# Performance work log

Hardware: AMD Instinct MI355X
Metric: run time of the kernel (lower is better)

## Reference

```python
import jax, jax.numpy as jnp
import numpy as np

LOG_CLAMP = -100.0  # torch BCELoss clamps log terms at -100


def setup_inputs() -> dict:
    key = jax.random.key(0)
    k1, k2 = jax.random.split(key)
    N, C, H, W = 32, 1, 1024, 1024
    # predict must be in (0,1) for BCE; keep strictly inside via small eps margin
    predict = jax.random.uniform(k1, (N, C, H, W), dtype=jnp.float32, minval=1e-6, maxval=1.0 - 1e-6)
    target = jax.random.uniform(k2, (N, C, H, W), dtype=jnp.float32)
    return {"predict": predict, "target": target}


def reference(predict, target):
    # Original loops over (b, row, col) and sums nn.BCELoss() (mean over the C
    # channel vector) per pixel. Equivalent fused form:
    #   loss = sum_{b,h,w} mean_c [ -(t*log(p) + (1-t)*log(1-p)) ]
    log_p = jnp.maximum(jnp.log(predict), LOG_CLAMP)
    log_1mp = jnp.maximum(jnp.log1p(-predict), LOG_CLAMP)
    bce = -(target * log_p + (1.0 - target) * log_1mp)  # [N, C, H, W]
    return bce.mean(axis=1).sum()
```

## Files before the change

kernel.cpp:

```cpp
#include <hip/hip_runtime.h>


#define NB  2048
#define BLK 256

#define LOG2_CLAMP -144.26950408889634f
#define NEG_LN2    -0.6931471805599453f

__device__ __forceinline__ float bce4_log2(float4 p, float4 t) {
    float s, lp, l1;
    lp = fmaxf(__log2f(p.x),        LOG2_CLAMP);
    l1 = fmaxf(__log2f(1.0f - p.x), LOG2_CLAMP);
    s  = l1 + t.x * (lp - l1);
    lp = fmaxf(__log2f(p.y),        LOG2_CLAMP);
    l1 = fmaxf(__log2f(1.0f - p.y), LOG2_CLAMP);
    s += l1 + t.y * (lp - l1);
    lp = fmaxf(__log2f(p.z),        LOG2_CLAMP);
    l1 = fmaxf(__log2f(1.0f - p.z), LOG2_CLAMP);
    s += l1 + t.z * (lp - l1);
    lp = fmaxf(__log2f(p.w),        LOG2_CLAMP);
    l1 = fmaxf(__log2f(1.0f - p.w), LOG2_CLAMP);
    s += l1 + t.w * (lp - l1);
    return s;
}

__device__ __forceinline__ float block_reduce(float acc) {
    #pragma unroll
    for (int off = 32; off > 0; off >>= 1)
        acc += __shfl_down(acc, off, 64);
    __shared__ float wave_sums[4];
    int lane = threadIdx.x & 63;
    int wave = threadIdx.x >> 6;
    if (lane == 0) wave_sums[wave] = acc;
    __syncthreads();
    float s = 0.0f;
    if (wave == 0) {
        s = (lane < 4) ? wave_sums[lane] : 0.0f;
        #pragma unroll
        for (int off = 2; off > 0; off >>= 1)
            s += __shfl_down(s, off, 64);
    }
    return s;
}

__global__ void __launch_bounds__(BLK) bce_partial_kernel(
        const float4* __restrict__ p4,
        const float4* __restrict__ t4,
        float* __restrict__ partials,
        int n4) {
    const int chunk = n4 / gridDim.x;
    const int base  = blockIdx.x * chunk;

    float a0 = 0.f, a1 = 0.f, a2 = 0.f, a3 = 0.f,
          a4 = 0.f, a5 = 0.f, a6 = 0.f, a7 = 0.f;

    int o = 0;
    for (; o + 8 * BLK <= chunk; o += 8 * BLK) {
        int i = base + o + threadIdx.x;
        float4 p0 = p4[i];           float4 p1 = p4[i + 1 * BLK];
        float4 p2 = p4[i + 2 * BLK]; float4 p3 = p4[i + 3 * BLK];
        float4 p4v = p4[i + 4 * BLK]; float4 p5 = p4[i + 5 * BLK];
        float4 p6 = p4[i + 6 * BLK]; float4 p7 = p4[i + 7 * BLK];
        float4 t0 = t4[i];           float4 t1 = t4[i + 1 * BLK];
        float4 t2 = t4[i + 2 * BLK]; float4 t3 = t4[i + 3 * BLK];
        float4 t4v = t4[i + 4 * BLK]; float4 t5 = t4[i + 5 * BLK];
        float4 t6 = t4[i + 6 * BLK]; float4 t7 = t4[i + 7 * BLK];
        a0 += bce4_log2(p0, t0);  a1 += bce4_log2(p1, t1);
        a2 += bce4_log2(p2, t2);  a3 += bce4_log2(p3, t3);
        a4 += bce4_log2(p4v, t4v); a5 += bce4_log2(p5, t5);
        a6 += bce4_log2(p6, t6);  a7 += bce4_log2(p7, t7);
    }
    for (; o < chunk; o += BLK) {
        int i = base + o + threadIdx.x;
        if (o + (int)threadIdx.x < chunk)
            a0 += bce4_log2(p4[i], t4[i]);
    }
    if (blockIdx.x == 0) {
        for (int i = (int)gridDim.x * chunk + threadIdx.x; i < n4; i += BLK)
            a0 += bce4_log2(p4[i], t4[i]);
    }

    float s = block_reduce(((a0 + a1) + (a2 + a3)) + ((a4 + a5) + (a6 + a7)));
    if (threadIdx.x == 0)
        partials[blockIdx.x] = NEG_LN2 * s;
}

__global__ void __launch_bounds__(BLK) bce_final_kernel(
        const float* __restrict__ partials,
        float* __restrict__ out,
        int nb) {
    float acc = 0.0f;
    for (int i = threadIdx.x; i < nb; i += BLK)
        acc += partials[i];
    float s = block_reduce(acc);
    if (threadIdx.x == 0)
        out[0] = s;
}

__global__ void __launch_bounds__(BLK) bce_atomic_kernel(
        const float4* __restrict__ p4,
        const float4* __restrict__ t4,
        float* __restrict__ out,
        int n4) {
    const int tid    = blockIdx.x * blockDim.x + threadIdx.x;
    const int stride = gridDim.x * blockDim.x;
    float a = 0.0f;
    for (int i = tid; i < n4; i += stride)
        a += bce4_log2(p4[i], t4[i]);
    float s = block_reduce(a);
    if (threadIdx.x == 0)
        atomicAdd(out, NEG_LN2 * s);
}

extern "C" void kernel_launch(void* const* d_in, const int* in_sizes, int n_in,
                              void* d_out, int out_size, void* d_ws, size_t ws_size,
                              hipStream_t stream) {
    const float* predict = (const float*)d_in[0];
    const float* target  = (const float*)d_in[1];
    float* out = (float*)d_out;

    int n  = in_sizes[0];
    int n4 = n / 4;

    if (ws_size >= NB * sizeof(float) && n4 >= NB) {
        float* partials = (float*)d_ws;
        bce_partial_kernel<<<NB, BLK, 0, stream>>>(
            (const float4*)predict, (const float4*)target, partials, n4);
        bce_final_kernel<<<1, BLK, 0, stream>>>(partials, out, NB);
    } else {
        hipMemsetAsync(d_out, 0, sizeof(float), stream);
        bce_atomic_kernel<<<NB, BLK, 0, stream>>>(
            (const float4*)predict, (const float4*)target, out, n4);
    }
}
```

Baseline: 47.46 us.

## Fuse final reduction into partial kernel via hierarchical last-block atomic counters

Replaces the separate single-block final reduction kernel with a last-block-done pattern. Each block writes its partial, fences, and increments a per-group counter; the last block of each group bumps a global counter, and the very last block sums all partials. This removes one kernel launch and the gap between kernels, but adds a memset of the counter area each call plus atomics and fences at the end of every block.

```diff
diff --git a/kernel.cpp b/kernel.cpp
--- a/kernel.cpp
+++ b/kernel.cpp
@@ -1,8 +1,10 @@
 #include <hip/hip_runtime.h>
 
 
-#define NB  2048
-#define BLK 256
+#define NB     2048
+#define BLK    256
+#define GROUPS 64
+#define GRP_SHIFT 5
 
 #define LOG2_CLAMP -144.26950408889634f
 #define NEG_LN2    -0.6931471805599453f
@@ -43,10 +45,12 @@
     return s;
 }
 
-__global__ void __launch_bounds__(BLK) bce_partial_kernel(
+__global__ void __launch_bounds__(BLK) bce_fused_kernel(
         const float4* __restrict__ p4,
         const float4* __restrict__ t4,
         float* __restrict__ partials,
+        int* __restrict__ counters,
+        float* __restrict__ out,
         int n4) {
     const int chunk = n4 / gridDim.x;
     const int base  = blockIdx.x * chunk;
@@ -57,18 +61,18 @@
     int o = 0;
     for (; o + 8 * BLK <= chunk; o += 8 * BLK) {
         int i = base + o + threadIdx.x;
-        float4 p0 = p4[i];           float4 p1 = p4[i + 1 * BLK];
-        float4 p2 = p4[i + 2 * BLK]; float4 p3 = p4[i + 3 * BLK];
+        float4 p0 = p4[i];            float4 p1 = p4[i + 1 * BLK];
+        float4 p2 = p4[i + 2 * BLK];  float4 p3 = p4[i + 3 * BLK];
         float4 p4v = p4[i + 4 * BLK]; float4 p5 = p4[i + 5 * BLK];
-        float4 p6 = p4[i + 6 * BLK]; float4 p7 = p4[i + 7 * BLK];
-        float4 t0 = t4[i];           float4 t1 = t4[i + 1 * BLK];
-        float4 t2 = t4[i + 2 * BLK]; float4 t3 = t4[i + 3 * BLK];
+        float4 p6 = p4[i + 6 * BLK];  float4 p7 = p4[i + 7 * BLK];
+        float4 t0 = t4[i];            float4 t1 = t4[i + 1 * BLK];
+        float4 t2 = t4[i + 2 * BLK];  float4 t3 = t4[i + 3 * BLK];
         float4 t4v = t4[i + 4 * BLK]; float4 t5 = t4[i + 5 * BLK];
-        float4 t6 = t4[i + 6 * BLK]; float4 t7 = t4[i + 7 * BLK];
-        a0 += bce4_log2(p0, t0);  a1 += bce4_log2(p1, t1);
-        a2 += bce4_log2(p2, t2);  a3 += bce4_log2(p3, t3);
+        float4 t6 = t4[i + 6 * BLK];  float4 t7 = t4[i + 7 * BLK];
+        a0 += bce4_log2(p0, t0);   a1 += bce4_log2(p1, t1);
+        a2 += bce4_log2(p2, t2);   a3 += bce4_log2(p3, t3);
         a4 += bce4_log2(p4v, t4v); a5 += bce4_log2(p5, t5);
-        a6 += bce4_log2(p6, t6);  a7 += bce4_log2(p7, t7);
+        a6 += bce4_log2(p6, t6);   a7 += bce4_log2(p7, t7);
     }
     for (; o < chunk; o += BLK) {
         int i = base + o + threadIdx.x;
@@ -81,20 +85,33 @@
     }
 
     float s = block_reduce(((a0 + a1) + (a2 + a3)) + ((a4 + a5) + (a6 + a7)));
-    if (threadIdx.x == 0)
+
+    __shared__ bool s_last;
+    if (threadIdx.x == 0) {
         partials[blockIdx.x] = NEG_LN2 * s;
-}
+        __threadfence();
+        bool last = false;
+        int g = blockIdx.x >> GRP_SHIFT;
+        int prev = __hip_atomic_fetch_add(&counters[g], 1,
+                       __ATOMIC_ACQ_REL, __HIP_MEMORY_SCOPE_AGENT);
+        if (prev == (NB / GROUPS) - 1) {
+            int prev2 = __hip_atomic_fetch_add(&counters[GROUPS], 1,
+                            __ATOMIC_ACQ_REL, __HIP_MEMORY_SCOPE_AGENT);
+            last = (prev2 == GROUPS - 1);
+        }
+        s_last = last;
+    }
+    __syncthreads();
 
-__global__ void __launch_bounds__(BLK) bce_final_kernel(
-        const float* __restrict__ partials,
-        float* __restrict__ out,
-        int nb) {
-    float acc = 0.0f;
-    for (int i = threadIdx.x; i < nb; i += BLK)
-        acc += partials[i];
-    float s = block_reduce(acc);
-    if (threadIdx.x == 0)
-        out[0] = s;
+    if (s_last) {
+        float acc = 0.0f;
+        for (int i = threadIdx.x; i < NB; i += BLK)
+            acc += __hip_atomic_load(&partials[i],
+                       __ATOMIC_RELAXED, __HIP_MEMORY_SCOPE_AGENT);
+        float r = block_reduce(acc);
+        if (threadIdx.x == 0)
+            out[0] = r;
+    }
 }
 
 __global__ void __launch_bounds__(BLK) bce_atomic_kernel(
@@ -122,11 +139,14 @@
     int n  = in_sizes[0];
     int n4 = n / 4;
 
-    if (ws_size >= NB * sizeof(float) && n4 >= NB) {
-        float* partials = (float*)d_ws;
-        bce_partial_kernel<<<NB, BLK, 0, stream>>>(
-            (const float4*)predict, (const float4*)target, partials, n4);
-        bce_final_kernel<<<1, BLK, 0, stream>>>(partials, out, NB);
+    const size_t need = 512 + (size_t)NB * sizeof(float);
+    if (ws_size >= need && n4 >= NB) {
+        int*   counters = (int*)d_ws;
+        float* partials = (float*)((char*)d_ws + 512);
+        hipMemsetAsync(d_ws, 0, 512, stream);
+        bce_fused_kernel<<<NB, BLK, 0, stream>>>(
+            (const float4*)predict, (const float4*)target,
+            partials, counters, out, n4);
     } else {
         hipMemsetAsync(d_out, 0, sizeof(float), stream);
         bce_atomic_kernel<<<NB, BLK, 0, stream>>>(
```

Result: slower. 179.7 us (+278.5%).
